# Kernel optimization log

Hardware: AMD Instinct MI355X
Metric: run time of the kernel (lower is better)

The kernel has to match this reference:

```python
import jax, jax.numpy as jnp
import numpy as np

N_SITES = 64   # number of sampled indices (n = 2**6 in source)
CHI = 64       # virtual bond dimension of the isometric TN
BATCH = 32768  # number of independent perfect samples


def _isometrize(W):
    """Right-canonical isometrization (analog of mera.isometrize(method='cayley')).

    W: [n, chi, 2, chi] raw params -> A with sum_{s,r} A[l,s,r] A[l',s,r] = delta_{ll'}.
    """
    n, chi = W.shape[0], W.shape[1]
    M = W.reshape(n, chi, 2 * chi)               # [n, chi, 2*chi]
    Q, _ = jnp.linalg.qr(jnp.swapaxes(M, 1, 2))  # [n, 2*chi, chi], orthonormal columns
    return jnp.swapaxes(Q, 1, 2).reshape(n, chi, 2, chi)


def setup_inputs() -> dict:
    key = jax.random.key(0)
    k1, k2 = jax.random.split(key)
    W = jax.random.normal(k1, (N_SITES, CHI, 2, CHI), dtype=jnp.float32)
    u = jax.random.uniform(k2, (BATCH, N_SITES), dtype=jnp.float32)
    return {"W": W, "u": u}


def reference(W, u):
    """Perfect (autoregressive exact-conditional) sampling from an isometric TN.

    Returns:
      s_hat: [B, n, 2] one-hot samples, outcome 0 -> [0,1], outcome 1 -> [1,0]
             (matching v0=[0,1], v1=[1,0] in the source)
      prob:  [B, n] conditional probability of the drawn outcome at each step
             (the `probability` array the source maintains).
    """
    A = _isometrize(W)                 # [n, chi, 2, chi]
    B, n = u.shape
    chi = W.shape[1]
    # left boundary environment (unit norm) -> total norm is exactly 1
    L0 = jnp.zeros((B, chi), dtype=W.dtype).at[:, 0].set(1.0)

    def step(L, inp):
        A_i, u_i = inp                              # [chi,2,chi], [B]
        T = jnp.einsum('bl,lsr->bsr', L, A_i)       # [B, 2, chi]
        p = jnp.sum(T * T, axis=-1)                 # [B, 2]; p0 + p1 == 1 by isometry
        take1 = u_i >= p[:, 0]                      # r < ps0 -> outcome 0
        s = take1.astype(jnp.int32)
        p_s = jnp.where(take1, p[:, 1], p[:, 0])    # probability of chosen branch
        T_s = jnp.where(take1[:, None], T[:, 1, :], T[:, 0, :])
        L_new = T_s / jnp.sqrt(p_s)[:, None]        # renormalize by sqrt(prob)
        return L_new, (s, p_s)

    _, (s, p) = jax.lax.scan(step, L0, (A, u.T))    # s,p: [n, B]
    s = s.T                                         # [B, n]
    prob = p.T                                      # [B, n]
    s_hat = jax.nn.one_hot(1 - s, 2, dtype=W.dtype)  # 0 -> [0,1], 1 -> [1,0]
    return s_hat, prob
```

## Files before the change

kernel.cpp:

```cpp
#include <hip/hip_runtime.h>

#define NSITES 64
#define CHI 64
#define BATCH 32768
#define LPAD 66

typedef double d4 __attribute__((ext_vector_type(4)));

#define MFMA_HAZARD_FENCE() do {                                    \
    __builtin_amdgcn_sched_barrier(0);                              \
    asm volatile("s_nop 7\n\ts_nop 7\n\ts_nop 7\n\ts_nop 7" :::);   \
    __builtin_amdgcn_sched_barrier(0);                              \
} while (0)

__global__ __launch_bounds__(512) void qr_site_kernel(
    const float* __restrict__ W, double* __restrict__ A8)
{
    __shared__ double M[128][65];
    __shared__ double wpart[8][64];
    __shared__ double tauS[64];
    __shared__ double redS[2];
    __shared__ double Vt[64][136];

    const int i   = blockIdx.x;
    const int tid = threadIdx.x;

    for (int idx = tid; idx < 8192; idx += 512) {
        int l = idx >> 7, sr = idx & 127;
        M[sr][l] = (double)W[i * 8192 + idx];
    }
    __syncthreads();

    const int jf = tid & 63;
    const int gf = tid >> 6;
    const int r0 = gf * 16;

    for (int k = 0; k < 64; ++k) {
        const double alpha = M[k][k];
        double v2 = 0.0;
        if (tid < 128) { double xv = (tid > k) ? M[tid][k] : 0.0; v2 = xv * xv; }
        #pragma unroll
        for (int off = 32; off; off >>= 1) v2 += __shfl_down(v2, off, 64);
        if (tid < 128 && (tid & 63) == 0) redS[tid >> 6] = v2;
        __syncthreads();
        const double xnorm2 = redS[0] + redS[1];

        double beta, tk;
        if (xnorm2 == 0.0) { beta = alpha; tk = 0.0; }
        else {
            double nrm = sqrt(alpha * alpha + xnorm2);
            beta = (alpha >= 0.0) ? -nrm : nrm;
            tk   = (beta - alpha) / beta;
        }
        const double sc = (tk != 0.0) ? (1.0 / (alpha - beta)) : 0.0;
        if (tid < 128 && tid > k && tk != 0.0) M[tid][k] *= sc;
        if (tid == 0) tauS[k] = tk;
        __syncthreads();

        double part = 0.0;
        if (jf > k) {
            #pragma unroll 4
            for (int m = 0; m < 16; ++m) {
                int rr = r0 + m;
                double vr = (rr > k) ? M[rr][k] : ((rr == k) ? 1.0 : 0.0);
                part = fma(vr, M[rr][jf], part);
            }
        }
        wpart[gf][jf] = part;
        __syncthreads();
        if (jf > k) {
            double wj = tauS[k] * (wpart[0][jf] + wpart[1][jf] + wpart[2][jf] + wpart[3][jf]
                                 + wpart[4][jf] + wpart[5][jf] + wpart[6][jf] + wpart[7][jf]);
            #pragma unroll 4
            for (int m = 0; m < 16; ++m) {
                int rr = r0 + m;
                double vr = (rr > k) ? M[rr][k] : ((rr == k) ? 1.0 : 0.0);
                M[rr][jf] = fma(-vr, wj, M[rr][jf]);
            }
        }
        __syncthreads();
    }

    for (int idx = tid; idx < 8192; idx += 512) {
        int rr = idx & 127, k = idx >> 7;
        double val = (rr > k) ? M[rr][k] : ((rr == k) ? 1.0 : 0.0);
        Vt[k][rr + (rr >> 4)] = val;
    }
    __syncthreads();

    const int jq = tid >> 3;
    const int qq = tid & 7;
    double E[16];
    #pragma unroll
    for (int m = 0; m < 16; ++m) E[m] = ((qq * 16 + m) == jq) ? 1.0 : 0.0;

    for (int k = 63; k >= 0; --k) {
        const double tkk = tauS[k];
        double part = 0.0;
        #pragma unroll
        for (int m = 0; m < 16; ++m) {
            int rr = qq * 16 + m;
            part = fma(Vt[k][rr + qq], E[m], part);
        }
        part += __shfl_xor(part, 1, 64);
        part += __shfl_xor(part, 2, 64);
        part += __shfl_xor(part, 4, 64);
        const double wj = tkk * part;
        #pragma unroll
        for (int m = 0; m < 16; ++m) {
            int rr = qq * 16 + m;
            E[m] = fma(-Vt[k][rr + qq], wj, E[m]);
        }
    }

    double* dst = A8 + (size_t)i * 8192 + jq * 128 + qq * 16;
    #pragma unroll
    for (int m = 0; m < 16; ++m) dst[m] = E[m];
}

#define MFMA_ROW(bp, a)                                                   \
    c0 = __builtin_amdgcn_mfma_f64_16x16x4f64((a), (bp)[  0], c0, 0,0,0); \
    c1 = __builtin_amdgcn_mfma_f64_16x16x4f64((a), (bp)[ 16], c1, 0,0,0); \
    c2 = __builtin_amdgcn_mfma_f64_16x16x4f64((a), (bp)[ 32], c2, 0,0,0); \
    c3 = __builtin_amdgcn_mfma_f64_16x16x4f64((a), (bp)[ 48], c3, 0,0,0); \
    c4 = __builtin_amdgcn_mfma_f64_16x16x4f64((a), (bp)[ 64], c4, 0,0,0); \
    c5 = __builtin_amdgcn_mfma_f64_16x16x4f64((a), (bp)[ 80], c5, 0,0,0); \
    c6 = __builtin_amdgcn_mfma_f64_16x16x4f64((a), (bp)[ 96], c6, 0,0,0); \
    c7 = __builtin_amdgcn_mfma_f64_16x16x4f64((a), (bp)[112], c7, 0,0,0);

__global__ __launch_bounds__(512, 2) void sample_kernel(
    const double* __restrict__ A8, const float* __restrict__ u,
    float* __restrict__ out)
{
    __shared__ __align__(16) double As[8192];
    __shared__ double Lsm[128 * LPAD];

    const int tid  = threadIdx.x;
    const int w    = tid >> 6;
    const int lane = tid & 63;
    const int g    = lane >> 4;
    const int r    = lane & 15;
    const int ubase = blockIdx.x * 128 + 16 * w;

    d4 zp = {0.0, 0.0, 0.0, 0.0};
    const d4 rowP = __builtin_amdgcn_mfma_f64_16x16x4f64((g == 0) ? (double)r : 0.0, 1.0, zp, 0, 0, 0);
    const d4 colP = __builtin_amdgcn_mfma_f64_16x16x4f64((g == 0) ? 1.0 : 0.0, (double)r, zp, 0, 0, 0);
    MFMA_HAZARD_FENCE();
    const int row0 = (int)(rowP.x + 0.5), row1 = (int)(rowP.y + 0.5);
    const int row2 = (int)(rowP.z + 0.5), row3 = (int)(rowP.w + 0.5);
    const int col0 = (int)(colP.x + 0.5), col1 = (int)(colP.y + 0.5);
    const int col2 = (int)(colP.z + 0.5), col3 = (int)(colP.w + 0.5);

    for (int j = g; j < 64; j += 4)
        Lsm[(16 * w + r) * LPAD + j] = (j == 0) ? 1.0 : 0.0;

    {
        const double2* s2 = (const double2*)A8;
        double2* a2 = (double2*)As;
        #pragma unroll
        for (int q = 0; q < 8; ++q) a2[q * 512 + tid] = s2[q * 512 + tid];
    }
    __syncthreads();

    float* probOut = out + (size_t)BATCH * (NSITES * 2);

    for (int site = 0; site < NSITES; ++site) {
        const float u0 = u[(size_t)(ubase + row0) * NSITES + site];
        const float u1 = u[(size_t)(ubase + row1) * NSITES + site];
        const float u2 = u[(size_t)(ubase + row2) * NSITES + site];
        const float u3 = u[(size_t)(ubase + row3) * NSITES + site];

        double2 st0, st1, st2, st3;
        if (site < NSITES - 1) {
            const double2* nx = (const double2*)(A8 + (size_t)(site + 1) * 8192);
            st0 = nx[0 * 512 + tid]; st1 = nx[1 * 512 + tid];
            st2 = nx[2 * 512 + tid]; st3 = nx[3 * 512 + tid];
        }

        d4 c0 = {0.0, 0.0, 0.0, 0.0}, c1 = c0, c2 = c0, c3 = c0;
        d4 c4 = c0, c5 = c0, c6 = c0, c7 = c0;

        const double* Lp = Lsm + (16 * w + r) * LPAD + g;
        const double* Ap = As + g * 128 + r;

        #pragma unroll
        for (int kk = 0; kk < 8; ++kk) {
            const double a = Lp[4 * kk];
            const double* bp = Ap + kk * 512;
            MFMA_ROW(bp, a)
        }

        __syncthreads();

        double2 st4, st5, st6, st7;
        if (site < NSITES - 1) {
            double2* a2 = (double2*)As;
            a2[0 * 512 + tid] = st0; a2[1 * 512 + tid] = st1;
            a2[2 * 512 + tid] = st2; a2[3 * 512 + tid] = st3;
            const double2* nx = (const double2*)(A8 + (size_t)(site + 1) * 8192);
            st4 = nx[4 * 512 + tid]; st5 = nx[5 * 512 + tid];
            st6 = nx[6 * 512 + tid]; st7 = nx[7 * 512 + tid];
        }

        #pragma unroll
        for (int kk = 8; kk < 16; ++kk) {
            const double a = Lp[4 * kk];
            const double* bp = Ap + kk * 512;
            MFMA_ROW(bp, a)
        }
        MFMA_HAZARD_FENCE();

        double P0 = fma(c3.x, c3.x, fma(c2.x, c2.x, fma(c1.x, c1.x, c0.x * c0.x)));
        double P1 = fma(c3.y, c3.y, fma(c2.y, c2.y, fma(c1.y, c1.y, c0.y * c0.y)));
        double P2 = fma(c3.z, c3.z, fma(c2.z, c2.z, fma(c1.z, c1.z, c0.z * c0.z)));
        double P3 = fma(c3.w, c3.w, fma(c2.w, c2.w, fma(c1.w, c1.w, c0.w * c0.w)));
        #pragma unroll
        for (int m = 1; m <= 8; m <<= 1) {
            P0 += __shfl_xor(P0, m, 64);
            P1 += __shfl_xor(P1, m, 64);
            P2 += __shfl_xor(P2, m, 64);
            P3 += __shfl_xor(P3, m, 64);
        }

        const bool t0 = ((double)u0 >= P0);
        const bool t1 = ((double)u1 >= P1);
        const bool t2 = ((double)u2 >= P2);
        const bool t3 = ((double)u3 >= P3);
        const double s0 = t0 ? (1.0 - P0) : P0;
        const double s1 = t1 ? (1.0 - P1) : P1;
        const double s2 = t2 ? (1.0 - P2) : P2;
        const double s3 = t3 ? (1.0 - P3) : P3;
        const double i0 = rsqrt(s0);
        const double i1 = rsqrt(s1);
        const double i2 = rsqrt(s2);
        const double i3 = rsqrt(s3);

        double* LwB = Lsm + (16 * w) * LPAD;
        LwB[row0 * LPAD +  0 + col0] = (t0 ? c4.x : c0.x) * i0;
        LwB[row0 * LPAD + 16 + col0] = (t0 ? c5.x : c1.x) * i0;
        LwB[row0 * LPAD + 32 + col0] = (t0 ? c6.x : c2.x) * i0;
        LwB[row0 * LPAD + 48 + col0] = (t0 ? c7.x : c3.x) * i0;
        LwB[row1 * LPAD +  0 + col1] = (t1 ? c4.y : c0.y) * i1;
        LwB[row1 * LPAD + 16 + col1] = (t1 ? c5.y : c1.y) * i1;
        LwB[row1 * LPAD + 32 + col1] = (t1 ? c6.y : c2.y) * i1;
        LwB[row1 * LPAD + 48 + col1] = (t1 ? c7.y : c3.y) * i1;
        LwB[row2 * LPAD +  0 + col2] = (t2 ? c4.z : c0.z) * i2;
        LwB[row2 * LPAD + 16 + col2] = (t2 ? c5.z : c1.z) * i2;
        LwB[row2 * LPAD + 32 + col2] = (t2 ? c6.z : c2.z) * i2;
        LwB[row2 * LPAD + 48 + col2] = (t2 ? c7.z : c3.z) * i2;
        LwB[row3 * LPAD +  0 + col3] = (t3 ? c4.w : c0.w) * i3;
        LwB[row3 * LPAD + 16 + col3] = (t3 ? c5.w : c1.w) * i3;
        LwB[row3 * LPAD + 32 + col3] = (t3 ? c6.w : c2.w) * i3;
        LwB[row3 * LPAD + 48 + col3] = (t3 ? c7.w : c3.w) * i3;

        if (r == 0) {
            probOut[(size_t)(ubase + row0) * NSITES + site] = (float)s0;
            probOut[(size_t)(ubase + row1) * NSITES + site] = (float)s1;
            probOut[(size_t)(ubase + row2) * NSITES + site] = (float)s2;
            probOut[(size_t)(ubase + row3) * NSITES + site] = (float)s3;
            *(float2*)(out + (size_t)(ubase + row0) * 128 + site * 2) = make_float2(t0 ? 1.f : 0.f, t0 ? 0.f : 1.f);
            *(float2*)(out + (size_t)(ubase + row1) * 128 + site * 2) = make_float2(t1 ? 1.f : 0.f, t1 ? 0.f : 1.f);
            *(float2*)(out + (size_t)(ubase + row2) * 128 + site * 2) = make_float2(t2 ? 1.f : 0.f, t2 ? 0.f : 1.f);
            *(float2*)(out + (size_t)(ubase + row3) * 128 + site * 2) = make_float2(t3 ? 1.f : 0.f, t3 ? 0.f : 1.f);
        }

        __syncthreads();

        if (site < NSITES - 1) {
            double2* a2 = (double2*)As;
            a2[4 * 512 + tid] = st4; a2[5 * 512 + tid] = st5;
            a2[6 * 512 + tid] = st6; a2[7 * 512 + tid] = st7;
        }
    }
}

extern "C" void kernel_launch(void* const* d_in, const int* in_sizes, int n_in,
                              void* d_out, int out_size, void* d_ws, size_t ws_size,
                              hipStream_t stream)
{
    const float* W = (const float*)d_in[0];
    const float* u = (const float*)d_in[1];
    float* out = (float*)d_out;
    double* A8 = (double*)d_ws;

    hipLaunchKernelGGL(qr_site_kernel, dim3(NSITES), dim3(512), 0, stream, W, A8);
    hipLaunchKernelGGL(sample_kernel, dim3(256), dim3(512), 0, stream, A8, u, out);
}
```

Measured before the change: 803.0 us.

## Fuse Householder norm and dot-product passes and defer reflector scaling

Each Householder step in the per-site QR kernel now computes the column norm and the projection w = vᵀM in one pass, using the unscaled column held in registers. The update is corrected analytically through tau/uk², and the reflector is normalised only when Vt is built. This removes one block-wide barrier and one shared-memory pass per column, at the cost of extra registers per thread. Row k of the R factor is no longer updated, which should not matter because only Q is consumed later.

```diff
diff --git a/kernel.cpp b/kernel.cpp
--- a/kernel.cpp
+++ b/kernel.cpp
@@ -19,7 +19,8 @@
     __shared__ double M[128][65];
     __shared__ double wpart[8][64];
     __shared__ double tauS[64];
-    __shared__ double redS[2];
+    __shared__ double scS[64];
+    __shared__ double redS2[8];
     __shared__ double Vt[64][136];
 
     const int i   = blockIdx.x;
@@ -29,53 +30,55 @@
         int l = idx >> 7, sr = idx & 127;
         M[sr][l] = (double)W[i * 8192 + idx];
     }
-    __syncthreads();
 
     const int jf = tid & 63;
     const int gf = tid >> 6;
     const int r0 = gf * 16;
+    __syncthreads();
 
     for (int k = 0; k < 64; ++k) {
+        double ureg[16];
+        #pragma unroll
+        for (int m = 0; m < 16; ++m) {
+            int rr = r0 + m;
+            ureg[m] = (rr > k) ? M[rr][k] : 0.0;
+        }
+        double np = 0.0;
+        #pragma unroll
+        for (int m = 0; m < 16; ++m) np = fma(ureg[m], ureg[m], np);
+        if (jf == 0) redS2[gf] = np;
+        if (jf > k) {
+            double part = 0.0;
+            #pragma unroll 4
+            for (int m = 0; m < 16; ++m)
+                part = fma(ureg[m], M[r0 + m][jf], part);
+            wpart[gf][jf] = part;
+        }
+        __syncthreads();
+
+        const double v2 = ((redS2[0] + redS2[1]) + (redS2[2] + redS2[3]))
+                        + ((redS2[4] + redS2[5]) + (redS2[6] + redS2[7]));
         const double alpha = M[k][k];
-        double v2 = 0.0;
-        if (tid < 128) { double xv = (tid > k) ? M[tid][k] : 0.0; v2 = xv * xv; }
-        #pragma unroll
-        for (int off = 32; off; off >>= 1) v2 += __shfl_down(v2, off, 64);
-        if (tid < 128 && (tid & 63) == 0) redS[tid >> 6] = v2;
-        __syncthreads();
-        const double xnorm2 = redS[0] + redS[1];
-
         double beta, tk;
-        if (xnorm2 == 0.0) { beta = alpha; tk = 0.0; }
+        if (v2 == 0.0) { beta = alpha; tk = 0.0; }
         else {
-            double nrm = sqrt(alpha * alpha + xnorm2);
+            double nrm = sqrt(alpha * alpha + v2);
             beta = (alpha >= 0.0) ? -nrm : nrm;
             tk   = (beta - alpha) / beta;
         }
-        const double sc = (tk != 0.0) ? (1.0 / (alpha - beta)) : 0.0;
-        if (tid < 128 && tid > k && tk != 0.0) M[tid][k] *= sc;
-        if (tid == 0) tauS[k] = tk;
-        __syncthreads();
-
-        double part = 0.0;
+        const double uk   = alpha - beta;
+        const double sc   = (tk != 0.0) ? (1.0 / uk) : 0.0;
+        const double tau2 = (tk != 0.0) ? (tk / (uk * uk)) : 0.0;
+        if (tid == 0) { tauS[k] = tk; scS[k] = sc; }
         if (jf > k) {
+            const double xk = M[k][jf];
+            double wsum = ((wpart[0][jf] + wpart[1][jf]) + (wpart[2][jf] + wpart[3][jf]))
+                        + ((wpart[4][jf] + wpart[5][jf]) + (wpart[6][jf] + wpart[7][jf]));
+            const double wj = tau2 * fma(uk, xk, wsum);
             #pragma unroll 4
             for (int m = 0; m < 16; ++m) {
                 int rr = r0 + m;
-                double vr = (rr > k) ? M[rr][k] : ((rr == k) ? 1.0 : 0.0);
-                part = fma(vr, M[rr][jf], part);
-            }
-        }
-        wpart[gf][jf] = part;
-        __syncthreads();
-        if (jf > k) {
-            double wj = tauS[k] * (wpart[0][jf] + wpart[1][jf] + wpart[2][jf] + wpart[3][jf]
-                                 + wpart[4][jf] + wpart[5][jf] + wpart[6][jf] + wpart[7][jf]);
-            #pragma unroll 4
-            for (int m = 0; m < 16; ++m) {
-                int rr = r0 + m;
-                double vr = (rr > k) ? M[rr][k] : ((rr == k) ? 1.0 : 0.0);
-                M[rr][jf] = fma(-vr, wj, M[rr][jf]);
+                M[rr][jf] = fma(-ureg[m], wj, M[rr][jf]);
             }
         }
         __syncthreads();
@@ -83,7 +86,7 @@
 
     for (int idx = tid; idx < 8192; idx += 512) {
         int rr = idx & 127, k = idx >> 7;
-        double val = (rr > k) ? M[rr][k] : ((rr == k) ? 1.0 : 0.0);
+        double val = (rr > k) ? M[rr][k] * scS[k] : ((rr == k) ? 1.0 : 0.0);
         Vt[k][rr + (rr >> 4)] = val;
     }
     __syncthreads();
```

New measurement: 753.6 us, median of 2. 1.07x faster.
